# Performance work log

Measured on AMD Instinct MI355X. Metric: run time of the kernel, lower is better.

The kernel has to match this reference:

```python
import jax, jax.numpy as jnp
import numpy as np

N_GENES = 2000
D_MODEL = 256
N_LAYERS = 4
D_STATE = 16
D_CONV = 4
EXPAND = 2
D_INNER = EXPAND * D_MODEL  # 512
DT_RANK = (D_MODEL + 15) // 16  # 16


def layer_norm(x, w, b, eps=1e-5):
    mu = jnp.mean(x, axis=-1, keepdims=True)
    var = jnp.mean((x - mu) ** 2, axis=-1, keepdims=True)
    return (x - mu) * jax.lax.rsqrt(var + eps) * w + b


def mamba_mixer(h, in_w, cw, cb, xp_w, dtp_w, dtp_b, A_log, Dvec, out_w):
    # h: [B, L, d_model]
    B, L, _ = h.shape
    xz = jnp.einsum('bld,ed->ble', h, in_w)            # [B,L,2*Di]
    u, z = jnp.split(xz, 2, axis=-1)                    # [B,L,Di] each
    # causal depthwise conv1d (kernel D_CONV)
    up = jnp.pad(u, ((0, 0), (D_CONV - 1, 0), (0, 0)))
    u = sum(up[:, k:k + L, :] * cw[:, k] for k in range(D_CONV)) + cb
    u = jax.nn.silu(u)
    # input-dependent dt, B, C
    xdbc = jnp.einsum('bld,ed->ble', u, xp_w)           # [B,L,dt_rank+2N]
    dt_r = xdbc[..., :DT_RANK]
    Bm = xdbc[..., DT_RANK:DT_RANK + D_STATE]           # [B,L,N]
    Cm = xdbc[..., DT_RANK + D_STATE:]                  # [B,L,N]
    dt = jax.nn.softplus(jnp.einsum('blr,dr->bld', dt_r, dtp_w) + dtp_b)  # [B,L,Di]
    A = -jnp.exp(A_log)                                 # [Di,N]
    dA = jnp.exp(dt[..., None] * A)                     # [B,L,Di,N]
    dBu = dt[..., None] * Bm[:, :, None, :] * u[..., None]

    def step(hst, inp):
        a, bu = inp
        hst = a * hst + bu
        return hst, hst

    h0 = jnp.zeros((B, D_INNER, D_STATE), dA.dtype)
    _, hs = jax.lax.scan(step, h0, (jnp.moveaxis(dA, 1, 0), jnp.moveaxis(dBu, 1, 0)))
    y = jnp.einsum('lbdn,lbn->bld', hs, jnp.moveaxis(Cm, 1, 0)) + u * Dvec
    y = y * jax.nn.silu(z)
    return jnp.einsum('bld,ed->ble', y, out_w)          # [B,L,d_model]


def setup_inputs() -> dict:
    key = jax.random.key(0)
    ks = jax.random.split(key, 16)
    nl = N_LAYERS
    inp = {
        'x': jax.random.normal(ks[0], (2, N_GENES), jnp.float32),
        'bulk_in_w': jax.random.normal(ks[1], (D_MODEL,), jnp.float32),
        'bulk_in_b': jnp.zeros((D_MODEL,), jnp.float32),
        'gene_emb': jax.random.normal(ks[2], (1, N_GENES, D_MODEL), jnp.float32) * 0.02,
        'mod_emb': jax.random.normal(ks[3], (1, 1, D_MODEL), jnp.float32) * 0.02,
        'ln_w': jnp.ones((nl, D_MODEL), jnp.float32),
        'ln_b': jnp.zeros((nl, D_MODEL), jnp.float32),
        'in_proj_w': jax.random.normal(ks[4], (nl, 2 * D_INNER, D_MODEL), jnp.float32) * (D_MODEL ** -0.5),
        'conv_w': jax.random.normal(ks[5], (nl, D_INNER, D_CONV), jnp.float32) * (D_CONV ** -0.5),
        'conv_b': jnp.zeros((nl, D_INNER), jnp.float32),
        'x_proj_w': jax.random.normal(ks[6], (nl, DT_RANK + 2 * D_STATE, D_INNER), jnp.float32) * (D_INNER ** -0.5),
        'dt_proj_w': jax.random.normal(ks[7], (nl, D_INNER, DT_RANK), jnp.float32) * 0.01,
        'dt_proj_b': jnp.full((nl, D_INNER), -4.0, jnp.float32),
        'A_log': jnp.broadcast_to(jnp.log(jnp.arange(1, D_STATE + 1, dtype=jnp.float32)), (nl, D_INNER, D_STATE)).copy(),
        'D': jnp.ones((nl, D_INNER), jnp.float32),
        'out_proj_w': jax.random.normal(ks[8], (nl, D_MODEL, D_INNER), jnp.float32) * (D_INNER ** -0.5),
        'fin_w': jnp.ones((D_MODEL,), jnp.float32),
        'fin_b': jnp.zeros((D_MODEL,), jnp.float32),
        'head_w': jax.random.normal(ks[9], (D_MODEL,), jnp.float32) * (D_MODEL ** -0.5),
        'head_b': jnp.zeros((), jnp.float32),
    }
    return inp


def reference(x, bulk_in_w, bulk_in_b, gene_emb, mod_emb, ln_w, ln_b, in_proj_w,
              conv_w, conv_b, x_proj_w, dt_proj_w, dt_proj_b, A_log, D, out_proj_w,
              fin_w, fin_b, head_w, head_b):
    # token embed (modality='bulk'); Linear(1,d_model) == x[...,None]*w + b
    h = x[..., None] * bulk_in_w + bulk_in_b + gene_emb + mod_emb  # [B,L,d_model]
    for i in range(N_LAYERS):
        h = h + mamba_mixer(layer_norm(h, ln_w[i], ln_b[i]), in_proj_w[i], conv_w[i],
                            conv_b[i], x_proj_w[i], dt_proj_w[i], dt_proj_b[i],
                            A_log[i], D[i], out_proj_w[i])
    h = layer_norm(h, fin_w, fin_b)
    y = jnp.einsum('bld,d->bl', h, head_w) + head_b  # bulk head, squeeze(-1)
    return y
```

## Files before the change

### kernel.cpp

```cpp
#include <hip/hip_runtime.h>
#include <math.h>

#define B_  2
#define L_  2000
#define DM_ 256
#define DI_ 512
#define DS_ 16
#define NL_ 4
#define BL_ (B_*L_)
#define BLP_ 4096
#define NC_  125
#define CL_  16
#define NST_ (B_*DI_*DS_)

typedef unsigned short ushort_t;
typedef __attribute__((ext_vector_type(8))) short bf16x8;
typedef __attribute__((ext_vector_type(4))) float f32x4;

__device__ __forceinline__ float siluf(float x) { return x / (1.f + __expf(-x)); }
__device__ __forceinline__ ushort_t f2bf(float x) {
    unsigned int u = __float_as_uint(x);
    return (ushort_t)((u + 0x7FFFu + ((u >> 16) & 1u)) >> 16);
}
__device__ __forceinline__ float bf2f(ushort_t v) {
    return __uint_as_float(((unsigned int)v) << 16);
}

__global__ __launch_bounds__(256) void embed_f2bf_kernel(
    const float* __restrict__ x, const float* __restrict__ biw,
    const float* __restrict__ bib, const float* __restrict__ ge,
    const float* __restrict__ me, const float* __restrict__ lnw,
    const float* __restrict__ lnb,
    float* __restrict__ h, ushort_t* __restrict__ aln,
    const float* __restrict__ s0, const float* __restrict__ s1,
    const float* __restrict__ s2, ushort_t* __restrict__ d0,
    ushort_t* __restrict__ d1, ushort_t* __restrict__ d2,
    int N0, int N1, int N2)
{
    if (blockIdx.x < BL_) {
        __shared__ float sm[8];
        int bl = blockIdx.x, d = threadIdx.x;
        int l = bl % L_;
        float v = x[bl]*biw[d] + bib[d] + ge[(size_t)l*DM_ + d] + me[d];
        h[(size_t)bl*DM_ + d] = v;
        float s = v, q = v*v;
        #pragma unroll
        for (int o = 32; o > 0; o >>= 1) {
            s += __shfl_down(s, o);
            q += __shfl_down(q, o);
        }
        if ((d & 63) == 0) { sm[d >> 6] = s; sm[4 + (d >> 6)] = q; }
        __syncthreads();
        float sum = sm[0]+sm[1]+sm[2]+sm[3];
        float ssq = sm[4]+sm[5]+sm[6]+sm[7];
        float mu  = sum * (1.f/DM_);
        float inv = rsqrtf(fmaxf(ssq*(1.f/DM_) - mu*mu, 0.f) + 1e-5f);
        aln[(size_t)bl*DM_ + d] = f2bf((v - mu)*inv*lnw[d] + lnb[d]);
    } else {
        int i = (blockIdx.x - BL_)*256 + threadIdx.x;
        const float* s; ushort_t* d; int j;
        if (i < N0)           { s = s0; d = d0; j = i; }
        else if (i < N0+N1)   { s = s1; d = d1; j = i - N0; }
        else if (i < N0+N1+N2){ s = s2; d = d2; j = i - N0 - N1; }
        else return;
        float4 v = *(const float4*)(s + 4*j);
        ushort_t o[4] = {f2bf(v.x), f2bf(v.y), f2bf(v.z), f2bf(v.w)};
        *(ushort2*)(d + 4*j)     = *(ushort2*)&o[0];
        *(ushort2*)(d + 4*j + 2) = *(ushort2*)&o[2];
    }
}

__global__ __launch_bounds__(256) void gemm_bf(
    const ushort_t* __restrict__ A, const ushort_t* __restrict__ W,
    ushort_t* __restrict__ C)
{
    __shared__ ushort_t a_s[128*64];
    __shared__ ushort_t b_s[128*64];
    const int r0 = blockIdx.x*128, c0 = blockIdx.y*128;
    const int tid = threadIdx.x;
    const int lane = tid & 63, w = tid >> 6;
    const int wm = (w & 1)*64, wn = (w >> 1)*64;
    const int qd = lane >> 4, l16 = lane & 15;
    f32x4 acc[4][4] = {};
    for (int kc = 0; kc < DM_; kc += 64) {
        #pragma unroll
        for (int q = 0; q < 4; q++) {
            int ch = tid + 256*q;
            int row = ch >> 3, col8 = (ch & 7)*8;
            *(bf16x8*)&a_s[row*64 + col8] =
                *(const bf16x8*)(A + (size_t)(r0 + row)*DM_ + kc + col8);
            *(bf16x8*)&b_s[row*64 + col8] =
                *(const bf16x8*)(W + (size_t)(c0 + row)*DM_ + kc + col8);
        }
        __syncthreads();
        #pragma unroll
        for (int ks = 0; ks < 2; ks++) {
            bf16x8 af[4], bf[4];
            #pragma unroll
            for (int i = 0; i < 4; i++)
                af[i] = *(const bf16x8*)&a_s[(wm + i*16 + l16)*64 + ks*32 + qd*8];
            #pragma unroll
            for (int j = 0; j < 4; j++)
                bf[j] = *(const bf16x8*)&b_s[(wn + j*16 + l16)*64 + ks*32 + qd*8];
            #pragma unroll
            for (int i = 0; i < 4; i++) {
                #pragma unroll
                for (int j = 0; j < 4; j++)
                    acc[i][j] = __builtin_amdgcn_mfma_f32_16x16x32_bf16(
                        af[i], bf[j], acc[i][j], 0, 0, 0);
            }
        }
        __syncthreads();
    }
    #pragma unroll
    for (int i = 0; i < 4; i++) {
        #pragma unroll
        for (int j = 0; j < 4; j++) {
            #pragma unroll
            for (int r = 0; r < 4; r++) {
                int row = r0 + wm + i*16 + qd*4 + r;
                int col = c0 + wn + j*16 + l16;
                C[(size_t)row*1024 + col] = f2bf(acc[i][j][r]);
            }
        }
    }
}

__global__ __launch_bounds__(512) void conv_xproj512(
    const ushort_t* __restrict__ xz, const float* __restrict__ cw,
    const float* __restrict__ cb, const ushort_t* __restrict__ XWb,
    const float* __restrict__ DTW, const float* __restrict__ DTB,
    const float* __restrict__ Alog,
    ushort_t* __restrict__ u_bf, float* __restrict__ bn,
    float* __restrict__ cn, ushort_t* __restrict__ dtn,
    float2* __restrict__ sa)
{
    __shared__ ushort_t xs[19][520];
    __shared__ ushort_t us[16][520];
    __shared__ float ps[8*768];
    __shared__ float dtr_s[16][16];
    const int c = blockIdx.x, b = blockIdx.y, l0 = c*CL_;
    const int tid = threadIdx.x;
    const int lane = tid & 63, w = tid >> 6;
    const int qd = lane >> 4, l16 = lane & 15;
    for (int f = tid; f < 19*64; f += 512) {
        int row = f >> 6, c8 = (f & 63)*8;
        int l = l0 - 3 + row;
        uint4 v = {0u,0u,0u,0u};
        if (l >= 0) v = *(const uint4*)(xz + (size_t)(b*L_ + l)*1024 + c8);
        *(uint4*)&xs[row][c8] = v;
    }
    __syncthreads();
    {
        int ch = tid;
        float4 wv = *(const float4*)(cw + ch*4);
        float bias = cb[ch];
        float x0 = bf2f(xs[0][ch]);
        float x1 = bf2f(xs[1][ch]);
        float x2 = bf2f(xs[2][ch]);
        #pragma unroll
        for (int j = 0; j < 16; j++) {
            float x3 = bf2f(xs[3 + j][ch]);
            float v = fmaf(x0, wv.x, fmaf(x1, wv.y, fmaf(x2, wv.z, fmaf(x3, wv.w, bias))));
            us[j][ch] = f2bf(siluf(v));
            x0 = x1; x1 = x2; x2 = x3;
        }
    }
    __syncthreads();
    for (int f = tid; f < 16*64; f += 512) {
        int row = f >> 6, c8 = (f & 63)*8;
        *(uint4*)(u_bf + (size_t)(b*L_ + l0 + row)*512 + c8) =
            *(const uint4*)&us[row][c8];
    }
    f32x4 acc[3] = {};
    #pragma unroll
    for (int st = 0; st < 2; st++) {
        int k = w*64 + st*32 + qd*8;
        bf16x8 af = *(const bf16x8*)&us[l16][k];
        #pragma unroll
        for (int j = 0; j < 3; j++) {
            bf16x8 bv = *(const bf16x8*)(XWb + (size_t)(j*16 + l16)*512 + k);
            acc[j] = __builtin_amdgcn_mfma_f32_16x16x32_bf16(af, bv, acc[j], 0, 0, 0);
        }
    }
    #pragma unroll
    for (int j = 0; j < 3; j++)
        #pragma unroll
        for (int r = 0; r < 4; r++)
            ps[w*768 + (qd*4 + r)*48 + j*16 + l16] = acc[j][r];
    __syncthreads();
    for (int e = tid; e < 768; e += 512) {
        float v = ps[e] + ps[768+e] + ps[1536+e] + ps[2304+e]
                + ps[3072+e] + ps[3840+e] + ps[4608+e] + ps[5376+e];
        ps[e] = v;
    }
    __syncthreads();
    if (tid < 256) {
        int row = tid >> 4, n = tid & 15;
        dtr_s[row][n] = ps[row*48 + n];
        size_t base = ((size_t)(b*L_) + l0 + row)*DS_ + n;
        bn[base] = ps[row*48 + 16 + n];
        cn[base] = ps[row*48 + 32 + n];
    }
    __syncthreads();
    {
        const int d = tid;
        float wreg[16];
        const float4* wp = (const float4*)(DTW + (size_t)d*16);
        #pragma unroll
        for (int k4 = 0; k4 < 4; k4++) {
            float4 v = wp[k4];
            wreg[4*k4+0] = v.x; wreg[4*k4+1] = v.y;
            wreg[4*k4+2] = v.z; wreg[4*k4+3] = v.w;
        }
        float bias = DTB[d];
        float dtv[16];
        #pragma unroll
        for (int r = 0; r < 16; r++) {
            float a = bias;
            #pragma unroll
            for (int k = 0; k < 16; k++) a = fmaf(dtr_s[r][k], wreg[k], a);
            float dt = a > 20.f ? a : log1pf(__expf(a));
            ushort_t dtb16 = f2bf(dt);
            dtn[((size_t)(b*L_) + l0 + r)*DI_ + d] = dtb16;
            dtv[r] = bf2f(dtb16);
        }
        float Ac[DS_], s[DS_], ap[DS_];
        const float* ar = Alog + (size_t)d*DS_;
        #pragma unroll
        for (int n = 0; n < DS_; n++) { Ac[n] = -__expf(ar[n]); s[n] = 0.f; ap[n] = 1.f; }
        #pragma unroll
        for (int l = 0; l < 16; l++) {
            float dt = dtv[l];
            float u  = bf2f(us[l][d]);
            float dtu = dt*u;
            #pragma unroll
            for (int n = 0; n < DS_; n++) {
                float e = __expf(dt*Ac[n]);
                s[n] = fmaf(e, s[n], dtu*ps[l*48 + 16 + n]);
                ap[n] *= e;
            }
        }
        size_t ib = (((size_t)c*B_ + b)*DI_ + d)*DS_;
        float2* sap = sa + ib;
        #pragma unroll
        for (int k = 0; k < 8; k++)
            *(float4*)&sap[2*k] = make_float4(s[2*k], ap[2*k], s[2*k+1], ap[2*k+1]);
    }
}

__global__ __launch_bounds__(64) void scan_phase2(
    const float2* __restrict__ sa, float* __restrict__ sinc)
{
    const int t = blockIdx.x*64 + threadIdx.x;
    float s = 0.f;
    for (int g = 0; g < 5; g++) {
        float2 v[25];
        #pragma unroll
        for (int i = 0; i < 25; i++)
            v[i] = sa[(size_t)(g*25 + i)*NST_ + t];
        #pragma unroll
        for (int i = 0; i < 25; i++) {
            sinc[(size_t)(g*25 + i)*NST_ + t] = s;
            s = fmaf(v[i].y, s, v[i].x);
        }
    }
}

template<int LAST>
__global__ __launch_bounds__(512) void phase3_fused(
    const ushort_t* __restrict__ dtn, const ushort_t* __restrict__ u_bf,
    const float* __restrict__ bn, const float* __restrict__ cn,
    const float* __restrict__ Alog, const float* __restrict__ Dv,
    const float* __restrict__ sinc, const ushort_t* __restrict__ xz,
    const ushort_t* __restrict__ opw, float* __restrict__ h,
    const float* __restrict__ lnw, const float* __restrict__ lnb,
    const ushort_t* __restrict__ ipw, ushort_t* __restrict__ xz_out,
    const float* __restrict__ hw, const float* __restrict__ hb,
    float* __restrict__ out)
{
    __shared__ float b_sh[CL_*DS_];
    __shared__ float c_sh[CL_*DS_];
    __shared__ ushort_t ys[16][520];
    __shared__ union { ushort_t dt_t[16][520]; ushort_t z_t[16][520]; } T0;
    __shared__ union { ushort_t u_t[16][520];  ushort_t a_sh[16][264]; } T1;
    __shared__ float2 red2[128];
    __shared__ float2 muv[16];
    const int c = blockIdx.x, b = blockIdx.y, l0 = c*CL_;
    const int tid = threadIdx.x;
    const int w = tid >> 6, lane = tid & 63;
    const int qd = lane >> 4, l16 = lane & 15;
    {
        int f = tid & 255;
        size_t src = ((size_t)(b*L_) + l0)*DS_ + f;
        if (tid < 256) b_sh[f] = bn[src];
        else           c_sh[f] = cn[src];
    }
    {
        const int r = tid >> 5, cb16 = (tid & 31)*16;
        size_t rb = ((size_t)(b*L_) + l0 + r)*DI_ + cb16;
        *(uint4*)&T0.dt_t[r][cb16]     = *(const uint4*)(dtn + rb);
        *(uint4*)&T0.dt_t[r][cb16 + 8] = *(const uint4*)(dtn + rb + 8);
        *(uint4*)&T1.u_t[r][cb16]      = *(const uint4*)(u_bf + rb);
        *(uint4*)&T1.u_t[r][cb16 + 8]  = *(const uint4*)(u_bf + rb + 8);
    }
    const int d = tid;
    float Ac[DS_], s[DS_];
    {
        const float* ar = Alog + (size_t)d*DS_;
        #pragma unroll
        for (int n = 0; n < DS_; n++) Ac[n] = -__expf(ar[n]);
        size_t base = (((size_t)c*B_ + b)*DI_ + d)*DS_;
        #pragma unroll
        for (int n4 = 0; n4 < 4; n4++)
            *(float4*)&s[4*n4] = *(const float4*)(sinc + base + 4*n4);
    }
    const float Dd = Dv[d];
    __syncthreads();
    float y_reg[CL_];
    #pragma unroll
    for (int l = 0; l < CL_; l++) {
        float dt = bf2f(T0.dt_t[l][d]);
        float u  = bf2f(T1.u_t[l][d]);
        float dtu = dt*u;
        float y = u*Dd;
        #pragma unroll
        for (int n = 0; n < DS_; n++) {
            float e = __expf(dt*Ac[n]);
            s[n] = fmaf(e, s[n], dtu*b_sh[l*DS_ + n]);
            y = fmaf(s[n], c_sh[l*DS_ + n], y);
        }
        y_reg[l] = y;
    }
    __syncthreads();
    {
        const int r = tid >> 5, cb16 = (tid & 31)*16;
        size_t rb = ((size_t)(b*L_) + l0 + r)*1024 + 512 + cb16;
        *(uint4*)&T0.z_t[r][cb16]     = *(const uint4*)(xz + rb);
        *(uint4*)&T0.z_t[r][cb16 + 8] = *(const uint4*)(xz + rb + 8);
    }
    __syncthreads();
    #pragma unroll
    for (int l = 0; l < CL_; l++)
        ys[l][d] = f2bf(y_reg[l] * siluf(bf2f(T0.z_t[l][d])));
    __syncthreads();
    f32x4 acc[2] = {};
    #pragma unroll
    for (int ks = 0; ks < 16; ks++) {
        bf16x8 af = *(const bf16x8*)&ys[l16][ks*32 + qd*8];
        #pragma unroll
        for (int j = 0; j < 2; j++) {
            bf16x8 bv = *(const bf16x8*)(opw + (size_t)(w*32 + j*16 + l16)*DI_ + ks*32 + qd*8);
            acc[j] = __builtin_amdgcn_mfma_f32_16x16x32_bf16(af, bv, acc[j], 0, 0, 0);
        }
    }
    float v[2][4];
    #pragma unroll
    for (int r = 0; r < 4; r++) {
        int lrow = qd*4 + r;
        size_t gr = (size_t)(b*L_ + l0 + lrow);
        float sm = 0.f, sq = 0.f;
        #pragma unroll
        for (int j = 0; j < 2; j++) {
            int col = w*32 + j*16 + l16;
            size_t idx = gr*DM_ + col;
            float vv = h[idx] + acc[j][r];
            if (!LAST) h[idx] = vv;
            v[j][r] = vv;
            sm += vv; sq += vv*vv;
        }
        sm += __shfl_xor(sm, 1); sq += __shfl_xor(sq, 1);
        sm += __shfl_xor(sm, 2); sq += __shfl_xor(sq, 2);
        sm += __shfl_xor(sm, 4); sq += __shfl_xor(sq, 4);
        sm += __shfl_xor(sm, 8); sq += __shfl_xor(sq, 8);
        if (l16 == 0) red2[w*16 + lrow] = make_float2(sm, sq);
    }
    __syncthreads();
    if (tid < 16) {
        float sm = 0.f, sq = 0.f;
        #pragma unroll
        for (int ww = 0; ww < 8; ww++) {
            float2 t = red2[ww*16 + tid];
            sm += t.x; sq += t.y;
        }
        float mu  = sm*(1.f/DM_);
        float inv = rsqrtf(fmaxf(sq*(1.f/DM_) - mu*mu, 0.f) + 1e-5f);
        muv[tid] = make_float2(mu, inv);
    }
    __syncthreads();
    if (!LAST) {
        #pragma unroll
        for (int r = 0; r < 4; r++) {
            int lrow = qd*4 + r;
            float2 mi = muv[lrow];
            #pragma unroll
            for (int j = 0; j < 2; j++) {
                int col = w*32 + j*16 + l16;
                T1.a_sh[lrow][col] = f2bf((v[j][r] - mi.x)*mi.y*lnw[col] + lnb[col]);
            }
        }
        __syncthreads();
        f32x4 acc2[8] = {};
        const int n0 = w*128;
        #pragma unroll
        for (int ks = 0; ks < 8; ks++) {
            bf16x8 af = *(const bf16x8*)&T1.a_sh[l16][ks*32 + qd*8];
            #pragma unroll
            for (int j2 = 0; j2 < 8; j2++) {
                bf16x8 bv = *(const bf16x8*)(ipw + (size_t)(n0 + j2*16 + l16)*DM_ + ks*32 + qd*8);
                acc2[j2] = __builtin_amdgcn_mfma_f32_16x16x32_bf16(af, bv, acc2[j2], 0, 0, 0);
            }
        }
        #pragma unroll
        for (int j2 = 0; j2 < 8; j2++) {
            #pragma unroll
            for (int r = 0; r < 4; r++) {
                size_t row = (size_t)(b*L_ + l0 + qd*4 + r);
                xz_out[row*1024 + n0 + j2*16 + l16] = f2bf(acc2[j2][r]);
            }
        }
    } else {
        float hd[4];
        #pragma unroll
        for (int r = 0; r < 4; r++) {
            int lrow = qd*4 + r;
            float2 mi = muv[lrow];
            float aa = 0.f;
            #pragma unroll
            for (int j = 0; j < 2; j++) {
                int col = w*32 + j*16 + l16;
                float nv = (v[j][r] - mi.x)*mi.y*lnw[col] + lnb[col];
                aa = fmaf(nv, hw[col], aa);
            }
            hd[r] = aa;
        }
        #pragma unroll
        for (int r = 0; r < 4; r++) {
            float xv = hd[r];
            xv += __shfl_xor(xv, 1); xv += __shfl_xor(xv, 2);
            xv += __shfl_xor(xv, 4); xv += __shfl_xor(xv, 8);
            if (l16 == 0) red2[w*16 + qd*4 + r].x = xv;
        }
        __syncthreads();
        if (tid < 16) {
            float xv = 0.f;
            #pragma unroll
            for (int ww = 0; ww < 8; ww++) xv += red2[ww*16 + tid].x;
            out[(size_t)(b*L_) + l0 + tid] = xv + hb[0];
        }
    }
}

extern "C" void kernel_launch(void* const* d_in, const int* in_sizes, int n_in,
                              void* d_out, int out_size, void* d_ws, size_t ws_size,
                              hipStream_t stream)
{
    const float* x    = (const float*)d_in[0];
    const float* biw  = (const float*)d_in[1];
    const float* bib  = (const float*)d_in[2];
    const float* ge   = (const float*)d_in[3];
    const float* me   = (const float*)d_in[4];
    const float* lnw  = (const float*)d_in[5];
    const float* lnb  = (const float*)d_in[6];
    const float* ipw  = (const float*)d_in[7];
    const float* cw   = (const float*)d_in[8];
    const float* cb   = (const float*)d_in[9];
    const float* xpw  = (const float*)d_in[10];
    const float* dtw  = (const float*)d_in[11];
    const float* dtb  = (const float*)d_in[12];
    const float* alog = (const float*)d_in[13];
    const float* Dv   = (const float*)d_in[14];
    const float* opw  = (const float*)d_in[15];
    const float* fw   = (const float*)d_in[16];
    const float* fb   = (const float*)d_in[17];
    const float* hw   = (const float*)d_in[18];
    const float* hb   = (const float*)d_in[19];
    float* out = (float*)d_out;

    float* ws  = (float*)d_ws;
    float* h      = ws;
    float* bn     = h + (size_t)BLP_*DM_;
    float* cn     = bn + (size_t)B_*L_*DS_;
    float2* sa    = (float2*)(cn + (size_t)B_*L_*DS_);
    float* sinc   = (float*)(sa + (size_t)NC_*NST_);
    ushort_t* aln   = (ushort_t*)(sinc + (size_t)NC_*NST_);
    ushort_t* xz_bf = aln + (size_t)BLP_*DM_;
    ushort_t* u_bf  = xz_bf + (size_t)BLP_*1024;
    ushort_t* dtn   = u_bf + (size_t)BLP_*DI_;
    ushort_t* ipwb  = dtn + (size_t)B_*L_*DI_;
    ushort_t* opwb  = ipwb + (size_t)NL_*1024*DM_;
    ushort_t* xpwb  = opwb + (size_t)NL_*DM_*DI_;

    const int N0 = NL_*1024*DM_/4, N1 = NL_*DM_*DI_/4, N2 = NL_*48*512/4;
    const int conv_blocks = (N0+N1+N2 + 255)/256;
    embed_f2bf_kernel<<<BL_ + conv_blocks, 256, 0, stream>>>(
        x, biw, bib, ge, me, lnw, lnb, h, aln,
        ipw, opw, xpw, ipwb, opwb, xpwb, N0, N1, N2);

    gemm_bf<<<dim3(BLP_/128, 1024/128), 256, 0, stream>>>(
        aln, ipwb, xz_bf);

    for (int i = 0; i < NL_; i++) {
        conv_xproj512<<<dim3(NC_, B_), 512, 0, stream>>>(
            xz_bf, cw + i*DI_*4, cb + i*DI_, xpwb + (size_t)i*48*512,
            dtw + (size_t)i*DI_*16, dtb + i*DI_, alog + (size_t)i*DI_*DS_,
            u_bf, bn, cn, dtn, sa);
        scan_phase2<<<NST_/64, 64, 0, stream>>>(sa, sinc);
        if (i < NL_-1) {
            phase3_fused<0><<<dim3(NC_, B_), 512, 0, stream>>>(
                dtn, u_bf, bn, cn, alog + (size_t)i*DI_*DS_, Dv + i*DI_,
                sinc, xz_bf, opwb + (size_t)i*DM_*DI_, h,
                lnw + (i+1)*DM_, lnb + (i+1)*DM_,
                ipwb + (size_t)(i+1)*1024*DM_, xz_bf,
                nullptr, nullptr, nullptr);
        } else {
            phase3_fused<1><<<dim3(NC_, B_), 512, 0, stream>>>(
                dtn, u_bf, bn, cn, alog + (size_t)i*DI_*DS_, Dv + i*DI_,
                sinc, xz_bf, opwb + (size_t)i*DM_*DI_, h,
                fw, fb,
                nullptr, xz_bf,
                hw, hb, out);
        }
    }
}
```

Before: 395.6 us.

## Fuse chunk-scan phase 2 into conv kernel via atomic ticket counter

Removes the separate scan_phase2 launch. Each conv_xproj block increments a per-layer atomic counter after writing its chunk state. The last 32 blocks to arrive spin until all 250 blocks are done and then run the inter-chunk prefix scan with 512 threads each. This saves a kernel launch and the gap between kernels. The cost is that the 32 tail blocks wait on the others, and the scheme only works if all 250 blocks can be resident at once; it relies on ticket ordering rather than a grid barrier.

```diff
diff --git a/kernel.cpp b/kernel.cpp
--- a/kernel.cpp
+++ b/kernel.cpp
@@ -12,6 +12,8 @@
 #define NC_  125
 #define CL_  16
 #define NST_ (B_*DI_*DS_)
+#define NCONVB_ 250
+#define NPH2B_  32
 
 typedef unsigned short ushort_t;
 typedef __attribute__((ext_vector_type(8))) short bf16x8;
@@ -35,7 +37,7 @@
     const float* __restrict__ s0, const float* __restrict__ s1,
     const float* __restrict__ s2, ushort_t* __restrict__ d0,
     ushort_t* __restrict__ d1, ushort_t* __restrict__ d2,
-    int N0, int N1, int N2)
+    int N0, int N1, int N2, unsigned int* __restrict__ cnt)
 {
     if (blockIdx.x < BL_) {
         __shared__ float sm[8];
@@ -57,6 +59,9 @@
         float inv = rsqrtf(fmaxf(ssq*(1.f/DM_) - mu*mu, 0.f) + 1e-5f);
         aln[(size_t)bl*DM_ + d] = f2bf((v - mu)*inv*lnw[d] + lnb[d]);
     } else {
+        if (blockIdx.x == BL_ && threadIdx.x < NL_)
+            __hip_atomic_store(&cnt[threadIdx.x], 0u,
+                               __ATOMIC_RELAXED, __HIP_MEMORY_SCOPE_AGENT);
         int i = (blockIdx.x - BL_)*256 + threadIdx.x;
         const float* s; ushort_t* d; int j;
         if (i < N0)           { s = s0; d = d0; j = i; }
@@ -133,12 +138,14 @@
     const float* __restrict__ Alog,
     ushort_t* __restrict__ u_bf, float* __restrict__ bn,
     float* __restrict__ cn, ushort_t* __restrict__ dtn,
-    float2* __restrict__ sa)
+    float2* __restrict__ sa, float* __restrict__ sinc,
+    unsigned int* __restrict__ cnt)
 {
     __shared__ ushort_t xs[19][520];
     __shared__ ushort_t us[16][520];
     __shared__ float ps[8*768];
     __shared__ float dtr_s[16][16];
+    __shared__ unsigned int tkt;
     const int c = blockIdx.x, b = blockIdx.y, l0 = c*CL_;
     const int tid = threadIdx.x;
     const int lane = tid & 63, w = tid >> 6;
@@ -247,22 +254,36 @@
         for (int k = 0; k < 8; k++)
             *(float4*)&sap[2*k] = make_float4(s[2*k], ap[2*k], s[2*k+1], ap[2*k+1]);
     }
-}
-
-__global__ __launch_bounds__(64) void scan_phase2(
-    const float2* __restrict__ sa, float* __restrict__ sinc)
-{
-    const int t = blockIdx.x*64 + threadIdx.x;
-    float s = 0.f;
-    for (int g = 0; g < 5; g++) {
-        float2 v[25];
-        #pragma unroll
-        for (int i = 0; i < 25; i++)
-            v[i] = sa[(size_t)(g*25 + i)*NST_ + t];
-        #pragma unroll
-        for (int i = 0; i < 25; i++) {
-            sinc[(size_t)(g*25 + i)*NST_ + t] = s;
-            s = fmaf(v[i].y, s, v[i].x);
+    asm volatile("s_waitcnt vmcnt(0)" ::: "memory");
+    __syncthreads();
+    if (tid == 0)
+        tkt = __hip_atomic_fetch_add(cnt, 1u, __ATOMIC_RELEASE,
+                                     __HIP_MEMORY_SCOPE_AGENT);
+    __syncthreads();
+    const unsigned int ticket = tkt;
+    if (ticket < NCONVB_ - NPH2B_) return;
+    if (tid == 0) {
+        while (__hip_atomic_load(cnt, __ATOMIC_ACQUIRE,
+                                 __HIP_MEMORY_SCOPE_AGENT) < (unsigned int)NCONVB_)
+            __builtin_amdgcn_s_sleep(16);
+    }
+    __syncthreads();
+    {
+        const int t = (int)(ticket - (NCONVB_ - NPH2B_))*512 + tid;
+        const unsigned long long* sap = (const unsigned long long*)sa;
+        float s = 0.f;
+        for (int g = 0; g < 5; g++) {
+            float2 v[25];
+            #pragma unroll
+            for (int i = 0; i < 25; i++)
+                v[i] = __builtin_bit_cast(float2,
+                    __hip_atomic_load(&sap[(size_t)(g*25 + i)*NST_ + t],
+                                      __ATOMIC_RELAXED, __HIP_MEMORY_SCOPE_AGENT));
+            #pragma unroll
+            for (int i = 0; i < 25; i++) {
+                sinc[(size_t)(g*25 + i)*NST_ + t] = s;
+                s = fmaf(v[i].y, s, v[i].x);
+            }
         }
     }
 }
@@ -490,12 +511,13 @@
     ushort_t* ipwb  = dtn + (size_t)B_*L_*DI_;
     ushort_t* opwb  = ipwb + (size_t)NL_*1024*DM_;
     ushort_t* xpwb  = opwb + (size_t)NL_*DM_*DI_;
+    unsigned int* cnt = (unsigned int*)(xpwb + (size_t)NL_*48*512);
 
     const int N0 = NL_*1024*DM_/4, N1 = NL_*DM_*DI_/4, N2 = NL_*48*512/4;
     const int conv_blocks = (N0+N1+N2 + 255)/256;
     embed_f2bf_kernel<<<BL_ + conv_blocks, 256, 0, stream>>>(
         x, biw, bib, ge, me, lnw, lnb, h, aln,
-        ipw, opw, xpw, ipwb, opwb, xpwb, N0, N1, N2);
+        ipw, opw, xpw, ipwb, opwb, xpwb, N0, N1, N2, cnt);
 
     gemm_bf<<<dim3(BLP_/128, 1024/128), 256, 0, stream>>>(
         aln, ipwb, xz_bf);
@@ -504,8 +526,7 @@
         conv_xproj512<<<dim3(NC_, B_), 512, 0, stream>>>(
             xz_bf, cw + i*DI_*4, cb + i*DI_, xpwb + (size_t)i*48*512,
             dtw + (size_t)i*DI_*16, dtb + i*DI_, alog + (size_t)i*DI_*DS_,
-            u_bf, bn, cn, dtn, sa);
-        scan_phase2<<<NST_/64, 64, 0, stream>>>(sa, sinc);
+            u_bf, bn, cn, dtn, sa, sinc, cnt + i);
         if (i < NL_-1) {
             phase3_fused<0><<<dim3(NC_, B_), 512, 0, stream>>>(
                 dtn, u_bf, bn, cn, alog + (size_t)i*DI_*DS_, Dv + i*DI_,
```

After: 508.5 us. +28.5%, slower.

## Fuse layer-0 in-projection GEMM into conv/x-proj chunk kernel

Applied to the files above, without the earlier changes.

Removes the standalone first-layer in_proj GEMM launch. It computes the projection per 16-token chunk inside the conv/x_proj kernel, with 3 extra halo rows. The u half stays in shared memory for the conv, and only the z half is written to global. This saves one launch and the round trip of the u half through global memory. In exchange, each block recomputes 3 halo rows, reads the weight matrix straight from global without shared-memory tiling, and the MFMA tiles are less efficient.

```diff
diff --git a/kernel.cpp b/kernel.cpp
--- a/kernel.cpp
+++ b/kernel.cpp
@@ -70,59 +70,164 @@
     }
 }
 
-__global__ __launch_bounds__(256) void gemm_bf(
-    const ushort_t* __restrict__ A, const ushort_t* __restrict__ W,
-    ushort_t* __restrict__ C)
+__global__ __launch_bounds__(512) void conv0_inproj(
+    const ushort_t* __restrict__ aln, const ushort_t* __restrict__ IPW,
+    ushort_t* __restrict__ xz,
+    const float* __restrict__ cw, const float* __restrict__ cb,
+    const ushort_t* __restrict__ XWb,
+    const float* __restrict__ DTW, const float* __restrict__ DTB,
+    const float* __restrict__ Alog,
+    ushort_t* __restrict__ u_bf, float* __restrict__ bn,
+    float* __restrict__ cn, ushort_t* __restrict__ dtn,
+    float2* __restrict__ sa)
 {
-    __shared__ ushort_t a_s[128*64];
-    __shared__ ushort_t b_s[128*64];
-    const int r0 = blockIdx.x*128, c0 = blockIdx.y*128;
+    __shared__ ushort_t xs[19][520];
+    __shared__ ushort_t us[16][520];
+    __shared__ union { float ps[8*768]; ushort_t als[32][264]; } U;
+    __shared__ float dtr_s[16][16];
+    const int c = blockIdx.x, b = blockIdx.y, l0 = c*CL_;
     const int tid = threadIdx.x;
     const int lane = tid & 63, w = tid >> 6;
-    const int wm = (w & 1)*64, wn = (w >> 1)*64;
     const int qd = lane >> 4, l16 = lane & 15;
-    f32x4 acc[4][4] = {};
-    for (int kc = 0; kc < DM_; kc += 64) {
-        #pragma unroll
-        for (int q = 0; q < 4; q++) {
-            int ch = tid + 256*q;
-            int row = ch >> 3, col8 = (ch & 7)*8;
-            *(bf16x8*)&a_s[row*64 + col8] =
-                *(const bf16x8*)(A + (size_t)(r0 + row)*DM_ + kc + col8);
-            *(bf16x8*)&b_s[row*64 + col8] =
-                *(const bf16x8*)(W + (size_t)(c0 + row)*DM_ + kc + col8);
-        }
-        __syncthreads();
-        #pragma unroll
-        for (int ks = 0; ks < 2; ks++) {
-            bf16x8 af[4], bf[4];
-            #pragma unroll
-            for (int i = 0; i < 4; i++)
-                af[i] = *(const bf16x8*)&a_s[(wm + i*16 + l16)*64 + ks*32 + qd*8];
-            #pragma unroll
-            for (int j = 0; j < 4; j++)
-                bf[j] = *(const bf16x8*)&b_s[(wn + j*16 + l16)*64 + ks*32 + qd*8];
-            #pragma unroll
-            for (int i = 0; i < 4; i++) {
-                #pragma unroll
-                for (int j = 0; j < 4; j++)
-                    acc[i][j] = __builtin_amdgcn_mfma_f32_16x16x32_bf16(
-                        af[i], bf[j], acc[i][j], 0, 0, 0);
+    {
+        int row = tid >> 4, c16 = (tid & 15)*16;
+        int gl = l0 - 3 + row;
+        uint4 v0 = {0u,0u,0u,0u}, v1 = {0u,0u,0u,0u};
+        if (row < 19 && gl >= 0) {
+            const ushort_t* p = aln + ((size_t)(b*L_ + gl))*DM_ + c16;
+            v0 = *(const uint4*)p;
+            v1 = *(const uint4*)(p + 8);
+        }
+        *(uint4*)&U.als[row][c16]     = v0;
+        *(uint4*)&U.als[row][c16 + 8] = v1;
+    }
+    __syncthreads();
+    const int n0 = w*128;
+    f32x4 accI[2][8] = {};
+    #pragma unroll
+    for (int ks = 0; ks < 8; ks++) {
+        bf16x8 af0 = *(const bf16x8*)&U.als[l16][ks*32 + qd*8];
+        bf16x8 af1 = *(const bf16x8*)&U.als[16 + l16][ks*32 + qd*8];
+        #pragma unroll
+        for (int j2 = 0; j2 < 8; j2++) {
+            bf16x8 bv = *(const bf16x8*)(IPW + (size_t)(n0 + j2*16 + l16)*DM_ + ks*32 + qd*8);
+            accI[0][j2] = __builtin_amdgcn_mfma_f32_16x16x32_bf16(af0, bv, accI[0][j2], 0, 0, 0);
+            accI[1][j2] = __builtin_amdgcn_mfma_f32_16x16x32_bf16(af1, bv, accI[1][j2], 0, 0, 0);
+        }
+    }
+    #pragma unroll
+    for (int m = 0; m < 2; m++) {
+        #pragma unroll
+        for (int j2 = 0; j2 < 8; j2++) {
+            #pragma unroll
+            for (int r = 0; r < 4; r++) {
+                int row_l = m*16 + qd*4 + r;
+                int col = n0 + j2*16 + l16;
+                ushort_t val = f2bf(accI[m][j2][r]);
+                if (col < 512) {
+                    if (row_l < 19) xs[row_l][col] = val;
+                } else if (row_l >= 3 && row_l < 19) {
+                    xz[((size_t)(b*L_ + l0 + row_l - 3))*1024 + col] = val;
+                }
             }
         }
-        __syncthreads();
-    }
-    #pragma unroll
-    for (int i = 0; i < 4; i++) {
-        #pragma unroll
-        for (int j = 0; j < 4; j++) {
-            #pragma unroll
-            for (int r = 0; r < 4; r++) {
-                int row = r0 + wm + i*16 + qd*4 + r;
-                int col = c0 + wn + j*16 + l16;
-                C[(size_t)row*1024 + col] = f2bf(acc[i][j][r]);
+    }
+    __syncthreads();
+    {
+        int ch = tid;
+        float4 wv = *(const float4*)(cw + ch*4);
+        float bias = cb[ch];
+        float x0 = bf2f(xs[0][ch]);
+        float x1 = bf2f(xs[1][ch]);
+        float x2 = bf2f(xs[2][ch]);
+        #pragma unroll
+        for (int j = 0; j < 16; j++) {
+            float x3 = bf2f(xs[3 + j][ch]);
+            float v = fmaf(x0, wv.x, fmaf(x1, wv.y, fmaf(x2, wv.z, fmaf(x3, wv.w, bias))));
+            us[j][ch] = f2bf(siluf(v));
+            x0 = x1; x1 = x2; x2 = x3;
+        }
+    }
+    __syncthreads();
+    for (int f = tid; f < 16*64; f += 512) {
+        int row = f >> 6, c8 = (f & 63)*8;
+        *(uint4*)(u_bf + (size_t)(b*L_ + l0 + row)*512 + c8) =
+            *(const uint4*)&us[row][c8];
+    }
+    f32x4 acc[3] = {};
+    #pragma unroll
+    for (int st = 0; st < 2; st++) {
+        int k = w*64 + st*32 + qd*8;
+        bf16x8 af = *(const bf16x8*)&us[l16][k];
+        #pragma unroll
+        for (int j = 0; j < 3; j++) {
+            bf16x8 bv = *(const bf16x8*)(XWb + (size_t)(j*16 + l16)*512 + k);
+            acc[j] = __builtin_amdgcn_mfma_f32_16x16x32_bf16(af, bv, acc[j], 0, 0, 0);
+        }
+    }
+    #pragma unroll
+    for (int j = 0; j < 3; j++)
+        #pragma unroll
+        for (int r = 0; r < 4; r++)
+            U.ps[w*768 + (qd*4 + r)*48 + j*16 + l16] = acc[j][r];
+    __syncthreads();
+    for (int e = tid; e < 768; e += 512) {
+        float v = U.ps[e] + U.ps[768+e] + U.ps[1536+e] + U.ps[2304+e]
+                + U.ps[3072+e] + U.ps[3840+e] + U.ps[4608+e] + U.ps[5376+e];
+        U.ps[e] = v;
+    }
+    __syncthreads();
+    if (tid < 256) {
+        int row = tid >> 4, n = tid & 15;
+        dtr_s[row][n] = U.ps[row*48 + n];
+        size_t base = ((size_t)(b*L_) + l0 + row)*DS_ + n;
+        bn[base] = U.ps[row*48 + 16 + n];
+        cn[base] = U.ps[row*48 + 32 + n];
+    }
+    __syncthreads();
+    {
+        const int d = tid;
+        float wreg[16];
+        const float4* wp = (const float4*)(DTW + (size_t)d*16);
+        #pragma unroll
+        for (int k4 = 0; k4 < 4; k4++) {
+            float4 v = wp[k4];
+            wreg[4*k4+0] = v.x; wreg[4*k4+1] = v.y;
+            wreg[4*k4+2] = v.z; wreg[4*k4+3] = v.w;
+        }
+        float bias = DTB[d];
+        float dtv[16];
+        #pragma unroll
+        for (int r = 0; r < 16; r++) {
+            float a = bias;
+            #pragma unroll
+            for (int k = 0; k < 16; k++) a = fmaf(dtr_s[r][k], wreg[k], a);
+            float dt = a > 20.f ? a : log1pf(__expf(a));
+            ushort_t dtb16 = f2bf(dt);
+            dtn[((size_t)(b*L_) + l0 + r)*DI_ + d] = dtb16;
+            dtv[r] = bf2f(dtb16);
+        }
+        float Ac[DS_], s[DS_], ap[DS_];
+        const float* ar = Alog + (size_t)d*DS_;
+        #pragma unroll
+        for (int n = 0; n < DS_; n++) { Ac[n] = -__expf(ar[n]); s[n] = 0.f; ap[n] = 1.f; }
+        #pragma unroll
+        for (int l = 0; l < 16; l++) {
+            float dt = dtv[l];
+            float u  = bf2f(us[l][d]);
+            float dtu = dt*u;
+            #pragma unroll
+            for (int n = 0; n < DS_; n++) {
+                float e = __expf(dt*Ac[n]);
+                s[n] = fmaf(e, s[n], dtu*U.ps[l*48 + 16 + n]);
+                ap[n] *= e;
             }
         }
+        size_t ib = (((size_t)c*B_ + b)*DI_ + d)*DS_;
+        float2* sap = sa + ib;
+        #pragma unroll
+        for (int k = 0; k < 8; k++)
+            *(float4*)&sap[2*k] = make_float4(s[2*k], ap[2*k], s[2*k+1], ap[2*k+1]);
     }
 }
 
@@ -497,14 +602,18 @@
         x, biw, bib, ge, me, lnw, lnb, h, aln,
         ipw, opw, xpw, ipwb, opwb, xpwb, N0, N1, N2);
 
-    gemm_bf<<<dim3(BLP_/128, 1024/128), 256, 0, stream>>>(
-        aln, ipwb, xz_bf);
-
     for (int i = 0; i < NL_; i++) {
-        conv_xproj512<<<dim3(NC_, B_), 512, 0, stream>>>(
-            xz_bf, cw + i*DI_*4, cb + i*DI_, xpwb + (size_t)i*48*512,
-            dtw + (size_t)i*DI_*16, dtb + i*DI_, alog + (size_t)i*DI_*DS_,
-            u_bf, bn, cn, dtn, sa);
+        if (i == 0) {
+            conv0_inproj<<<dim3(NC_, B_), 512, 0, stream>>>(
+                aln, ipwb, xz_bf,
+                cw, cb, xpwb, dtw, dtb, alog,
+                u_bf, bn, cn, dtn, sa);
+        } else {
+            conv_xproj512<<<dim3(NC_, B_), 512, 0, stream>>>(
+                xz_bf, cw + i*DI_*4, cb + i*DI_, xpwb + (size_t)i*48*512,
+                dtw + (size_t)i*DI_*16, dtb + i*DI_, alog + (size_t)i*DI_*DS_,
+                u_bf, bn, cn, dtn, sa);
+        }
         scan_phase2<<<NST_/64, 64, 0, stream>>>(sa, sinc);
         if (i < NL_-1) {
             phase3_fused<0><<<dim3(NC_, B_), 512, 0, stream>>>(
```

Result: no change. 400.7 us (+1.3%).

## Pre-pack bf16 weights into MFMA fragment order for coalesced B loads

Applied to the files above, without the earlier changes.

The fp32-to-bf16 weight conversion now writes in_proj, out_proj and x_proj weights in a per-lane MFMA fragment order, so each wave's B-operand load is one contiguous 1 KB read. The first in_proj GEMM drops its B shared-memory tile and reads fragments straight from global memory. The conv/x_proj, out_proj and fused in_proj paths are rewritten to the same packed indexing. This is meant to remove strided, uncoalesced weight loads and LDS staging, at the cost of more complex index math in the conversion pass and B reads that now depend on cache hits.

```diff
diff --git a/kernel.cpp b/kernel.cpp
--- a/kernel.cpp
+++ b/kernel.cpp
@@ -13,6 +13,11 @@
 #define CL_  16
 #define NST_ (B_*DI_*DS_)
 
+#define NF_IP_ (NL_*64*8*64)
+#define NF_OP_ (NL_*16*16*64)
+#define NF_XP_ (NL_*3*16*64)
+#define NF_TOT_ (NF_IP_ + NF_OP_ + NF_XP_)
+
 typedef unsigned short ushort_t;
 typedef __attribute__((ext_vector_type(8))) short bf16x8;
 typedef __attribute__((ext_vector_type(4))) float f32x4;
@@ -32,10 +37,9 @@
     const float* __restrict__ me, const float* __restrict__ lnw,
     const float* __restrict__ lnb,
     float* __restrict__ h, ushort_t* __restrict__ aln,
-    const float* __restrict__ s0, const float* __restrict__ s1,
-    const float* __restrict__ s2, ushort_t* __restrict__ d0,
-    ushort_t* __restrict__ d1, ushort_t* __restrict__ d2,
-    int N0, int N1, int N2)
+    const float* __restrict__ ipw, const float* __restrict__ opw,
+    const float* __restrict__ xpw, ushort_t* __restrict__ ipwb,
+    ushort_t* __restrict__ opwb, ushort_t* __restrict__ xpwb)
 {
     if (blockIdx.x < BL_) {
         __shared__ float sm[8];
@@ -58,29 +62,62 @@
         aln[(size_t)bl*DM_ + d] = f2bf((v - mu)*inv*lnw[d] + lnb[d]);
     } else {
         int i = (blockIdx.x - BL_)*256 + threadIdx.x;
-        const float* s; ushort_t* d; int j;
-        if (i < N0)           { s = s0; d = d0; j = i; }
-        else if (i < N0+N1)   { s = s1; d = d1; j = i - N0; }
-        else if (i < N0+N1+N2){ s = s2; d = d2; j = i - N0 - N1; }
-        else return;
-        float4 v = *(const float4*)(s + 4*j);
-        ushort_t o[4] = {f2bf(v.x), f2bf(v.y), f2bf(v.z), f2bf(v.w)};
-        *(ushort2*)(d + 4*j)     = *(ushort2*)&o[0];
-        *(ushort2*)(d + 4*j + 2) = *(ushort2*)&o[2];
+        if (i >= NF_TOT_) return;
+        const float* src; ushort_t* dst;
+        if (i < NF_IP_) {
+            int f = i;
+            int li   = f >> 15;
+            int r    = f & 32767;
+            int t    = r >> 9;
+            int rem  = r & 511;
+            int ks   = rem >> 6;
+            int lane = rem & 63;
+            src = ipw + ((size_t)(li*1024 + t*16 + (lane & 15)))*DM_
+                      + ks*32 + (lane >> 4)*8;
+            dst = ipwb + (size_t)f*8;
+        } else if (i < NF_IP_ + NF_OP_) {
+            int f = i - NF_IP_;
+            int li   = f >> 14;
+            int r    = f & 16383;
+            int t    = r >> 10;
+            int rem  = r & 1023;
+            int ks   = rem >> 6;
+            int lane = rem & 63;
+            src = opw + ((size_t)(li*256 + t*16 + (lane & 15)))*DI_
+                      + ks*32 + (lane >> 4)*8;
+            dst = opwb + (size_t)f*8;
+        } else {
+            int f = i - NF_IP_ - NF_OP_;
+            int li   = f / 3072;
+            int r    = f % 3072;
+            int t    = r >> 10;
+            int rem  = r & 1023;
+            int ks   = rem >> 6;
+            int lane = rem & 63;
+            src = xpw + ((size_t)(li*48 + t*16 + (lane & 15)))*DI_
+                      + ks*32 + (lane >> 4)*8;
+            dst = xpwb + (size_t)f*8;
+        }
+        float4 v0 = *(const float4*)src;
+        float4 v1 = *(const float4*)(src + 4);
+        __align__(16) ushort_t o[8];
+        o[0] = f2bf(v0.x); o[1] = f2bf(v0.y); o[2] = f2bf(v0.z); o[3] = f2bf(v0.w);
+        o[4] = f2bf(v1.x); o[5] = f2bf(v1.y); o[6] = f2bf(v1.z); o[7] = f2bf(v1.w);
+        *(uint4*)dst = *(const uint4*)o;
     }
 }
 
 __global__ __launch_bounds__(256) void gemm_bf(
-    const ushort_t* __restrict__ A, const ushort_t* __restrict__ W,
+    const ushort_t* __restrict__ A, const ushort_t* __restrict__ Wp,
     ushort_t* __restrict__ C)
 {
     __shared__ ushort_t a_s[128*64];
-    __shared__ ushort_t b_s[128*64];
     const int r0 = blockIdx.x*128, c0 = blockIdx.y*128;
     const int tid = threadIdx.x;
     const int lane = tid & 63, w = tid >> 6;
     const int wm = (w & 1)*64, wn = (w >> 1)*64;
     const int qd = lane >> 4, l16 = lane & 15;
+    const int tb = (c0 + wn) >> 4;
     f32x4 acc[4][4] = {};
     for (int kc = 0; kc < DM_; kc += 64) {
         #pragma unroll
@@ -89,19 +126,19 @@
             int row = ch >> 3, col8 = (ch & 7)*8;
             *(bf16x8*)&a_s[row*64 + col8] =
                 *(const bf16x8*)(A + (size_t)(r0 + row)*DM_ + kc + col8);
-            *(bf16x8*)&b_s[row*64 + col8] =
-                *(const bf16x8*)(W + (size_t)(c0 + row)*DM_ + kc + col8);
         }
         __syncthreads();
         #pragma unroll
         for (int ks = 0; ks < 2; ks++) {
+            int ksg = (kc >> 5) + ks;
             bf16x8 af[4], bf[4];
             #pragma unroll
             for (int i = 0; i < 4; i++)
                 af[i] = *(const bf16x8*)&a_s[(wm + i*16 + l16)*64 + ks*32 + qd*8];
             #pragma unroll
             for (int j = 0; j < 4; j++)
-                bf[j] = *(const bf16x8*)&b_s[(wn + j*16 + l16)*64 + ks*32 + qd*8];
+                bf[j] = *(const bf16x8*)(Wp +
+                    (((size_t)(tb + j)*8 + ksg)*64 + lane)*8);
             #pragma unroll
             for (int i = 0; i < 4; i++) {
                 #pragma unroll
@@ -128,7 +165,7 @@
 
 __global__ __launch_bounds__(512) void conv_xproj512(
     const ushort_t* __restrict__ xz, const float* __restrict__ cw,
-    const float* __restrict__ cb, const ushort_t* __restrict__ XWb,
+    const float* __restrict__ cb, const ushort_t* __restrict__ XWp,
     const float* __restrict__ DTW, const float* __restrict__ DTB,
     const float* __restrict__ Alog,
     ushort_t* __restrict__ u_bf, float* __restrict__ bn,
@@ -176,10 +213,12 @@
     #pragma unroll
     for (int st = 0; st < 2; st++) {
         int k = w*64 + st*32 + qd*8;
+        int ksg = w*2 + st;
         bf16x8 af = *(const bf16x8*)&us[l16][k];
         #pragma unroll
         for (int j = 0; j < 3; j++) {
-            bf16x8 bv = *(const bf16x8*)(XWb + (size_t)(j*16 + l16)*512 + k);
+            bf16x8 bv = *(const bf16x8*)(XWp +
+                (((size_t)j*16 + ksg)*64 + lane)*8);
             acc[j] = __builtin_amdgcn_mfma_f32_16x16x32_bf16(af, bv, acc[j], 0, 0, 0);
         }
     }
@@ -350,7 +389,8 @@
         bf16x8 af = *(const bf16x8*)&ys[l16][ks*32 + qd*8];
         #pragma unroll
         for (int j = 0; j < 2; j++) {
-            bf16x8 bv = *(const bf16x8*)(opw + (size_t)(w*32 + j*16 + l16)*DI_ + ks*32 + qd*8);
+            bf16x8 bv = *(const bf16x8*)(opw +
+                (((size_t)(w*2 + j)*16 + ks)*64 + lane)*8);
             acc[j] = __builtin_amdgcn_mfma_f32_16x16x32_bf16(af, bv, acc[j], 0, 0, 0);
         }
     }
@@ -407,7 +447,8 @@
             bf16x8 af = *(const bf16x8*)&T1.a_sh[l16][ks*32 + qd*8];
             #pragma unroll
             for (int j2 = 0; j2 < 8; j2++) {
-                bf16x8 bv = *(const bf16x8*)(ipw + (size_t)(n0 + j2*16 + l16)*DM_ + ks*32 + qd*8);
+                bf16x8 bv = *(const bf16x8*)(ipw +
+                    (((size_t)(w*8 + j2)*8 + ks)*64 + lane)*8);
                 acc2[j2] = __builtin_amdgcn_mfma_f32_16x16x32_bf16(af, bv, acc2[j2], 0, 0, 0);
             }
         }
@@ -491,11 +532,10 @@
     ushort_t* opwb  = ipwb + (size_t)NL_*1024*DM_;
     ushort_t* xpwb  = opwb + (size_t)NL_*DM_*DI_;
 
-    const int N0 = NL_*1024*DM_/4, N1 = NL_*DM_*DI_/4, N2 = NL_*48*512/4;
-    const int conv_blocks = (N0+N1+N2 + 255)/256;
+    const int conv_blocks = (NF_TOT_ + 255)/256;
     embed_f2bf_kernel<<<BL_ + conv_blocks, 256, 0, stream>>>(
         x, biw, bib, ge, me, lnw, lnb, h, aln,
-        ipw, opw, xpw, ipwb, opwb, xpwb, N0, N1, N2);
+        ipw, opw, xpw, ipwb, opwb, xpwb);
 
     gemm_bf<<<dim3(BLP_/128, 1024/128), 256, 0, stream>>>(
         aln, ipwb, xz_bf);
```

New measurement: 354.9 us (median of 2 runs). 10.3% less time.
